# Kernel tuning notes

Hardware: AMD Instinct MI355X
Metric: run time of the kernel (lower is better)

## Reference

```python
import jax, jax.numpy as jnp
import numpy as np

SQRT_HALF = 1.0 / np.sqrt(2.0)


def _sep_filter(x, h, axis):
    """Depthwise 1D filter along `axis` (-1 = rows of the image i.e. horizontal,
    -2 = columns i.e. vertical) with symmetric boundary extension.
    x: (B, C, H, W); h: (m,) with m odd. Output has same spatial shape.
    Matches torch F.conv2d (cross-correlation) with groups=C on symmetric-padded input."""
    ch = x.shape[1]
    m = h.shape[0]
    p = m // 2
    if axis == -1:
        xe = jnp.pad(x, ((0, 0), (0, 0), (0, 0), (p, p)), mode='symmetric')
        k = jnp.tile(h.reshape(1, 1, 1, m), (ch, 1, 1, 1))
    else:
        xe = jnp.pad(x, ((0, 0), (0, 0), (p, p), (0, 0)), mode='symmetric')
        k = jnp.tile(h.reshape(1, 1, m, 1), (ch, 1, 1, 1))
    return jax.lax.conv_general_dilated(
        xe, k, window_strides=(1, 1), padding='VALID',
        dimension_numbers=('NCHW', 'OIHW', 'NCHW'), feature_group_count=ch)


def rowfilter(x, h):
    return _sep_filter(x, h, axis=-1)


def colfilter(x, h):
    return _sep_filter(x, h, axis=-2)


def q2c(y):
    """Quads -> two complex subimages. Returns (z1r, z1i, z2r, z2i),
    each (B, C, H/2, W/2)."""
    y = y * SQRT_HALF
    a = y[..., 0::2, 0::2]
    b = y[..., 0::2, 1::2]
    c = y[..., 1::2, 0::2]
    d = y[..., 1::2, 1::2]
    return a - d, b + c, a + d, b - c


def setup_inputs() -> dict:
    key = jax.random.key(0)
    k1, k2, k3 = jax.random.split(key, 3)
    B, C, H, W = 4, 32, 512, 512
    x = jax.random.normal(k1, (B, C, H, W), dtype=jnp.float32)
    h0o = jax.random.normal(k2, (5,), dtype=jnp.float32)  # near_sym_a lowpass: 5 taps
    h1o = jax.random.normal(k3, (7,), dtype=jnp.float32)  # near_sym_a highpass: 7 taps
    return {"input": x, "h0o": h0o, "h1o": h1o}


def reference(input, h0o, h1o):
    Lo = rowfilter(input, h0o)
    Hi = rowfilter(input, h1o)
    LoLo = colfilter(Lo, h0o)
    LoHi = colfilter(Lo, h1o)
    HiLo = colfilter(Hi, h0o)
    HiHi = colfilter(Hi, h1o)

    deg15r, deg15i, deg165r, deg165i = q2c(LoHi)
    deg45r, deg45i, deg135r, deg135i = q2c(HiHi)
    deg75r, deg75i, deg105r, deg105i = q2c(HiLo)

    Yhr = jnp.stack([deg15r, deg45r, deg75r, deg105r, deg135r, deg165r], axis=2)
    Yhi = jnp.stack([deg15i, deg45i, deg75i, deg105i, deg135i, deg165i], axis=2)
    Yl = LoLo
    return Yl, Yhr, Yhi
```

## Files before the change

### kernel.cpp

```cpp
#include <hip/hip_runtime.h>

#define H 512
#define W 512
#define NIMG 128
#define TH 16
#define TW 128
#define XR (TH + 6)
#define XC 136
#define XFLAT (XR * XC)
#define XPAD 3072
#define YSPLIT 4
#define NT (H / TH / YSPLIT)

#define YHR_OFF ((long)NIMG * H * W)
#define BSTRIDE ((long)(H / 2) * (W / 2))
#define YH_SIZE ((long)NIMG * 6 * BSTRIDE)
#define YHI_OFF (YHR_OFF + YH_SIZE)

__device__ __forceinline__ int reflect512(int g) {
    g = (g < 0) ? (-1 - g) : g;
    g = (g > H - 1) ? (2 * H - 1 - g) : g;
    return g;
}

__device__ __forceinline__ float4 f4fma(float s, float4 a, float4 acc) {
    acc.x = fmaf(s, a.x, acc.x);
    acc.y = fmaf(s, a.y, acc.y);
    acc.z = fmaf(s, a.z, acc.z);
    acc.w = fmaf(s, a.w, acc.w);
    return acc;
}

__global__ __launch_bounds__(256, 4)
void dtcwt_fwd1(const float* __restrict__ x,
                const float* __restrict__ h0o,
                const float* __restrict__ h1o,
                float* __restrict__ out)
{
    __shared__ __align__(16) float xin[XPAD];
    __shared__ __align__(16) float slo[XR][TW];
    __shared__ __align__(16) float shi[XR][TW];

    const int tid = threadIdx.x;
    const int x0 = blockIdx.x * TW;
    const int ys = blockIdx.y * (NT * TH);
    const int img = blockIdx.z;

    float c0[5], c1[7];
#pragma unroll
    for (int j = 0; j < 5; ++j) c0[j] = h0o[j];
#pragma unroll
    for (int j = 0; j < 7; ++j) c1[j] = h1o[j];

    const long ibase = (long)img * (H * W);
    float* __restrict__ yhr = out + YHR_OFF;
    float* __restrict__ yhi = out + YHI_OFF;
    const float sc = 0.70710678118654752440f;

    int sr[3]; int sst[3]; bool srev[3]; bool sact[3];
#pragma unroll
    for (int s = 0; s < 3; ++s) {
        int flat = tid * 4 + s * 1024;
        sact[s] = (flat < XFLAT);
        int r = flat / XC;
        int c = flat - r * XC;
        int g0 = x0 - 4 + c;
        int st = g0; bool rv = false;
        if (g0 < 0)          { st = -g0 - 4;        rv = true; }
        else if (g0 > W - 4) { st = 2 * W - 4 - g0; rv = true; }
        sr[s] = r; sst[s] = st; srev[s] = rv;
    }

    auto stage_issue = [&](int t, float4 v[3]) {
        const int yb = ys + t * TH - 3;
#pragma unroll
        for (int s = 0; s < 3; ++s) {
            if (!sact[s]) continue;
            const int gy = reflect512(yb + sr[s]);
            v[s] = *(const float4*)&x[ibase + (long)gy * W + sst[s]];
        }
    };
    auto stage_write = [&](float4 v[3]) {
#pragma unroll
        for (int s = 0; s < 3; ++s) {
            if (!sact[s]) continue;
            float4 w = v[s];
            if (srev[s]) w = make_float4(w.w, w.z, w.y, w.x);
            *(float4*)&xin[tid * 4 + s * 1024] = w;
        }
    };

    {
        float4 stg[3];
        stage_issue(0, stg);
        stage_write(stg);
    }
    __syncthreads();

    for (int t = 0; t < NT; ++t) {
        float4 nstg[3];
        if (t + 1 < NT) stage_issue(t + 1, nstg);

        for (int i = tid; i < XR * (TW / 4); i += 256) {
            int r = i >> 5;
            int w0 = (i & 31) * 4;
            const float* xr = &xin[r * XC];
            float4 A  = *(const float4*)&xr[w0];
            float4 Bv = *(const float4*)&xr[w0 + 4];
            float4 Cv = *(const float4*)&xr[w0 + 8];
            float f1 = A.y, f2 = A.z, f3 = A.w;
            float f4 = Bv.x, f5 = Bv.y, f6 = Bv.z, f7 = Bv.w;
            float f8 = Cv.x, f9 = Cv.y, f10 = Cv.z;
            float lo0 = c0[0]*f2 + c0[1]*f3 + c0[2]*f4 + c0[3]*f5 + c0[4]*f6;
            float lo1 = c0[0]*f3 + c0[1]*f4 + c0[2]*f5 + c0[3]*f6 + c0[4]*f7;
            float lo2 = c0[0]*f4 + c0[1]*f5 + c0[2]*f6 + c0[3]*f7 + c0[4]*f8;
            float lo3 = c0[0]*f5 + c0[1]*f6 + c0[2]*f7 + c0[3]*f8 + c0[4]*f9;
            float hi0 = c1[0]*f1 + c1[1]*f2 + c1[2]*f3 + c1[3]*f4 + c1[4]*f5 + c1[5]*f6 + c1[6]*f7;
            float hi1 = c1[0]*f2 + c1[1]*f3 + c1[2]*f4 + c1[3]*f5 + c1[4]*f6 + c1[5]*f7 + c1[6]*f8;
            float hi2 = c1[0]*f3 + c1[1]*f4 + c1[2]*f5 + c1[3]*f6 + c1[4]*f7 + c1[5]*f8 + c1[6]*f9;
            float hi3 = c1[0]*f4 + c1[1]*f5 + c1[2]*f6 + c1[3]*f7 + c1[4]*f8 + c1[5]*f9 + c1[6]*f10;
            *(float4*)&slo[r][w0] = make_float4(lo0, lo1, lo2, lo3);
            *(float4*)&shi[r][w0] = make_float4(hi0, hi1, hi2, hi3);
        }
        __syncthreads();

        {
            const int qr = tid >> 5;
            const int q4 = tid & 31;
            const int r0 = qr * 2;
            const int w0 = q4 * 4;
            const int yt = ys + t * TH;

            float4 L[8];
#pragma unroll
            for (int j = 0; j < 8; ++j) L[j] = *(const float4*)&slo[r0 + j][w0];

            float4 ll0 = make_float4(0.f, 0.f, 0.f, 0.f);
            float4 ll1 = ll0, lh0 = ll0, lh1 = ll0;
#pragma unroll
            for (int j = 0; j < 5; ++j) {
                ll0 = f4fma(c0[j], L[1 + j], ll0);
                ll1 = f4fma(c0[j], L[2 + j], ll1);
            }
#pragma unroll
            for (int j = 0; j < 7; ++j) {
                lh0 = f4fma(c1[j], L[j],     lh0);
                lh1 = f4fma(c1[j], L[1 + j], lh1);
            }

            const long ylb = ibase + (long)(yt + r0) * W + (x0 + w0);
            *(float4*)&out[ylb]     = ll0;
            *(float4*)&out[ylb + W] = ll1;

            float4 Hv[8];
#pragma unroll
            for (int j = 0; j < 8; ++j) Hv[j] = *(const float4*)&shi[r0 + j][w0];

            float4 hl0 = make_float4(0.f, 0.f, 0.f, 0.f);
            float4 hl1 = hl0, hh0 = hl0, hh1 = hl0;
#pragma unroll
            for (int j = 0; j < 5; ++j) {
                hl0 = f4fma(c0[j], Hv[1 + j], hl0);
                hl1 = f4fma(c0[j], Hv[2 + j], hl1);
            }
#pragma unroll
            for (int j = 0; j < 7; ++j) {
                hh0 = f4fma(c1[j], Hv[j],     hh0);
                hh1 = f4fma(c1[j], Hv[1 + j], hh1);
            }

            const int qy = (yt >> 1) + qr;
            const int qx = (x0 >> 1) + q4 * 2;
            const long hb = (long)img * 6 * BSTRIDE + (long)qy * (W / 2) + qx;

            *(float2*)&yhr[hb + 0 * BSTRIDE] = make_float2((lh0.x - lh1.y) * sc, (lh0.z - lh1.w) * sc);
            *(float2*)&yhi[hb + 0 * BSTRIDE] = make_float2((lh0.y + lh1.x) * sc, (lh0.w + lh1.z) * sc);
            *(float2*)&yhr[hb + 1 * BSTRIDE] = make_float2((hh0.x - hh1.y) * sc, (hh0.z - hh1.w) * sc);
            *(float2*)&yhi[hb + 1 * BSTRIDE] = make_float2((hh0.y + hh1.x) * sc, (hh0.w + hh1.z) * sc);
            *(float2*)&yhr[hb + 2 * BSTRIDE] = make_float2((hl0.x - hl1.y) * sc, (hl0.z - hl1.w) * sc);
            *(float2*)&yhi[hb + 2 * BSTRIDE] = make_float2((hl0.y + hl1.x) * sc, (hl0.w + hl1.z) * sc);
            *(float2*)&yhr[hb + 3 * BSTRIDE] = make_float2((hl0.x + hl1.y) * sc, (hl0.z + hl1.w) * sc);
            *(float2*)&yhi[hb + 3 * BSTRIDE] = make_float2((hl0.y - hl1.x) * sc, (hl0.w - hl1.z) * sc);
            *(float2*)&yhr[hb + 4 * BSTRIDE] = make_float2((hh0.x + hh1.y) * sc, (hh0.z + hh1.w) * sc);
            *(float2*)&yhi[hb + 4 * BSTRIDE] = make_float2((hh0.y - hh1.x) * sc, (hh0.w - hh1.z) * sc);
            *(float2*)&yhr[hb + 5 * BSTRIDE] = make_float2((lh0.x + lh1.y) * sc, (lh0.z + lh1.w) * sc);
            *(float2*)&yhi[hb + 5 * BSTRIDE] = make_float2((lh0.y - lh1.x) * sc, (lh0.w - lh1.z) * sc);
        }

        if (t + 1 < NT) stage_write(nstg);
        __syncthreads();
    }
}

extern "C" void kernel_launch(void* const* d_in, const int* in_sizes, int n_in,
                              void* d_out, int out_size, void* d_ws, size_t ws_size,
                              hipStream_t stream) {
    const float* x   = (const float*)d_in[0];
    const float* h0o = (const float*)d_in[1];
    const float* h1o = (const float*)d_in[2];
    float* out = (float*)d_out;
    dim3 grid(W / TW, YSPLIT, NIMG);
    dtcwt_fwd1<<<grid, dim3(256), 0, stream>>>(x, h0o, h1o, out);
}
```

Measured before the change: 662.5 us.

## Stage input tiles with direct global-to-LDS loads and separate halo buffer

Replaces register-staged float4 loads of the input tile with global_load_lds DMA into a dense interior LDS buffer, and loads the reflected horizontal halo separately as scalars into a small halo array. The next tile's interior load is issued after the row-filter sync so it overlaps with the column-filter and output-store phase. This removes register staging and the reversal shuffles for boundary chunks, but adds branchy halo selection in the row filter and relies on the async LDS writes completing before the end-of-iteration barrier (no explicit vmcnt wait is visible).

```diff
diff --git a/kernel.cpp b/kernel.cpp
--- a/kernel.cpp
+++ b/kernel.cpp
@@ -6,11 +6,11 @@
 #define TH 16
 #define TW 128
 #define XR (TH + 6)
-#define XC 136
-#define XFLAT (XR * XC)
-#define XPAD 3072
 #define YSPLIT 4
 #define NT (H / TH / YSPLIT)
+
+#define NCHUNK (XR * (TW / 4))
+#define NHALO  (XR * 8)
 
 #define YHR_OFF ((long)NIMG * H * W)
 #define BSTRIDE ((long)(H / 2) * (W / 2))
@@ -31,13 +31,18 @@
     return acc;
 }
 
+#define GLOAD_LDS16(g, l) __builtin_amdgcn_global_load_lds(                      \
+    (const __attribute__((address_space(1))) void*)(g),                          \
+    (__attribute__((address_space(3))) void*)(l), 16, 0, 0)
+
 __global__ __launch_bounds__(256, 4)
 void dtcwt_fwd1(const float* __restrict__ x,
                 const float* __restrict__ h0o,
                 const float* __restrict__ h1o,
                 float* __restrict__ out)
 {
-    __shared__ __align__(16) float xin[XPAD];
+    __shared__ __align__(16) float xint[XR][TW];
+    __shared__ __align__(16) float xhalo[XR][8];
     __shared__ __align__(16) float slo[XR][TW];
     __shared__ __align__(16) float shi[XR][TW];
 
@@ -57,57 +62,49 @@
     float* __restrict__ yhi = out + YHI_OFF;
     const float sc = 0.70710678118654752440f;
 
-    int sr[3]; int sst[3]; bool srev[3]; bool sact[3];
+    int   sr[3]; int sgx[3]; bool sact[3]; float* sdst[3];
 #pragma unroll
     for (int s = 0; s < 3; ++s) {
-        int flat = tid * 4 + s * 1024;
-        sact[s] = (flat < XFLAT);
-        int r = flat / XC;
-        int c = flat - r * XC;
-        int g0 = x0 - 4 + c;
-        int st = g0; bool rv = false;
-        if (g0 < 0)          { st = -g0 - 4;        rv = true; }
-        else if (g0 > W - 4) { st = 2 * W - 4 - g0; rv = true; }
-        sr[s] = r; sst[s] = st; srev[s] = rv;
+        int k = tid + 256 * s;
+        sact[s] = (k < NCHUNK);
+        sr[s]   = k >> 5;
+        sgx[s]  = x0 + 4 * (k & 31);
+        sdst[s] = &xint[0][0] + k * 4;
     }
-
-    auto stage_issue = [&](int t, float4 v[3]) {
+    const bool hact0 = (tid < NHALO);
+    const int  hr = tid >> 3;
+    const int  hj = tid & 7;
+    const int  hgx = reflect512((hj < 4) ? (x0 - 4 + hj) : (x0 + 124 + hj));
+
+    auto issue_interior = [&](int t) {
         const int yb = ys + t * TH - 3;
 #pragma unroll
         for (int s = 0; s < 3; ++s) {
             if (!sact[s]) continue;
             const int gy = reflect512(yb + sr[s]);
-            v[s] = *(const float4*)&x[ibase + (long)gy * W + sst[s]];
+            GLOAD_LDS16(&x[ibase + (long)gy * W + sgx[s]], sdst[s]);
         }
     };
-    auto stage_write = [&](float4 v[3]) {
-#pragma unroll
-        for (int s = 0; s < 3; ++s) {
-            if (!sact[s]) continue;
-            float4 w = v[s];
-            if (srev[s]) w = make_float4(w.w, w.z, w.y, w.x);
-            *(float4*)&xin[tid * 4 + s * 1024] = w;
-        }
-    };
-
-    {
-        float4 stg[3];
-        stage_issue(0, stg);
-        stage_write(stg);
-    }
+
+    issue_interior(0);
+    if (hact0) xhalo[hr][hj] = x[ibase + (long)reflect512(ys - 3 + hr) * W + hgx];
     __syncthreads();
 
     for (int t = 0; t < NT; ++t) {
-        float4 nstg[3];
-        if (t + 1 < NT) stage_issue(t + 1, nstg);
+        const bool hact = hact0 && (t + 1 < NT);
+        float hreg = 0.f;
+        if (hact)
+            hreg = x[ibase + (long)reflect512(ys + (t + 1) * TH - 3 + hr) * W + hgx];
 
         for (int i = tid; i < XR * (TW / 4); i += 256) {
             int r = i >> 5;
             int w0 = (i & 31) * 4;
-            const float* xr = &xin[r * XC];
-            float4 A  = *(const float4*)&xr[w0];
-            float4 Bv = *(const float4*)&xr[w0 + 4];
-            float4 Cv = *(const float4*)&xr[w0 + 8];
+            const float* rowi = &xint[r][0];
+            const float* pa = (w0 == 0)   ? &xhalo[r][0] : rowi + (w0 - 4);
+            const float* pc = (w0 == 124) ? &xhalo[r][4] : rowi + (w0 + 4);
+            float4 A  = *(const float4*)pa;
+            float4 Bv = *(const float4*)(rowi + w0);
+            float4 Cv = *(const float4*)pc;
             float f1 = A.y, f2 = A.z, f3 = A.w;
             float f4 = Bv.x, f5 = Bv.y, f6 = Bv.z, f7 = Bv.w;
             float f8 = Cv.x, f9 = Cv.y, f10 = Cv.z;
@@ -124,6 +121,11 @@
         }
         __syncthreads();
 
+        if (t + 1 < NT) {
+            issue_interior(t + 1);
+            if (hact) xhalo[hr][hj] = hreg;
+        }
+
         {
             const int qr = tid >> 5;
             const int q4 = tid & 31;
@@ -187,7 +189,6 @@
             *(float2*)&yhi[hb + 5 * BSTRIDE] = make_float2((lh0.y - lh1.x) * sc, (lh0.w - lh1.z) * sc);
         }
 
-        if (t + 1 < NT) stage_write(nstg);
         __syncthreads();
     }
 }
```

Measured after the change: 626.6 us. -5.4%, faster.

## Replace shared-memory tiling with register sliding window over full-width rows

Applied to the files above, without the earlier changes.

Each 128-thread block now covers a full 512-wide row band, and each thread holds an 8-row ring buffer of row-filtered results in registers. Rows are streamed in with global float4 loads, neighbour columns are read straight from global or L1, and the two edge threads handle mirror boundaries. This drops shared memory and all __syncthreads, and cuts the vertical halo overhead by using taller bands. In exchange it uses more registers, has less parallelism (16x128 blocks of 128 threads), does redundant neighbour loads, and relies on the compiler keeping the ring-buffer indexing in registers after full unrolling.

```diff
diff --git a/kernel.cpp b/kernel.cpp
--- a/kernel.cpp
+++ b/kernel.cpp
@@ -3,14 +3,8 @@
 #define H 512
 #define W 512
 #define NIMG 128
-#define TH 16
-#define TW 128
-#define XR (TH + 6)
-#define XC 136
-#define XFLAT (XR * XC)
-#define XPAD 3072
-#define YSPLIT 4
-#define NT (H / TH / YSPLIT)
+#define NBAND 16
+#define BR (H / NBAND)
 
 #define YHR_OFF ((long)NIMG * H * W)
 #define BSTRIDE ((long)(H / 2) * (W / 2))
@@ -31,20 +25,33 @@
     return acc;
 }
 
-__global__ __launch_bounds__(256, 4)
+__device__ __forceinline__ void rowcomp(float4 A, float4 Bv, float4 C,
+                                        const float* c0, const float* c1,
+                                        float4& lo, float4& hi) {
+    float f1 = A.y, f2 = A.z, f3 = A.w;
+    float f4 = Bv.x, f5 = Bv.y, f6 = Bv.z, f7 = Bv.w;
+    float f8 = C.x, f9 = C.y, f10 = C.z;
+    lo.x = c0[0]*f2 + c0[1]*f3 + c0[2]*f4 + c0[3]*f5 + c0[4]*f6;
+    lo.y = c0[0]*f3 + c0[1]*f4 + c0[2]*f5 + c0[3]*f6 + c0[4]*f7;
+    lo.z = c0[0]*f4 + c0[1]*f5 + c0[2]*f6 + c0[3]*f7 + c0[4]*f8;
+    lo.w = c0[0]*f5 + c0[1]*f6 + c0[2]*f7 + c0[3]*f8 + c0[4]*f9;
+    hi.x = c1[0]*f1 + c1[1]*f2 + c1[2]*f3 + c1[3]*f4 + c1[4]*f5 + c1[5]*f6 + c1[6]*f7;
+    hi.y = c1[0]*f2 + c1[1]*f3 + c1[2]*f4 + c1[3]*f5 + c1[4]*f6 + c1[5]*f7 + c1[6]*f8;
+    hi.z = c1[0]*f3 + c1[1]*f4 + c1[2]*f5 + c1[3]*f6 + c1[4]*f7 + c1[5]*f8 + c1[6]*f9;
+    hi.w = c1[0]*f4 + c1[1]*f5 + c1[2]*f6 + c1[3]*f7 + c1[4]*f8 + c1[5]*f9 + c1[6]*f10;
+}
+
+__global__ __launch_bounds__(128, 3)
 void dtcwt_fwd1(const float* __restrict__ x,
                 const float* __restrict__ h0o,
                 const float* __restrict__ h1o,
                 float* __restrict__ out)
 {
-    __shared__ __align__(16) float xin[XPAD];
-    __shared__ __align__(16) float slo[XR][TW];
-    __shared__ __align__(16) float shi[XR][TW];
-
-    const int tid = threadIdx.x;
-    const int x0 = blockIdx.x * TW;
-    const int ys = blockIdx.y * (NT * TH);
-    const int img = blockIdx.z;
+    const int t   = threadIdx.x;
+    const int cg  = t * 4;
+    const int ys  = blockIdx.x * BR;
+    const int img = blockIdx.y;
+    const bool e0 = (t == 0), e1 = (t == 127);
 
     float c0[5], c1[7];
 #pragma unroll
@@ -53,142 +60,105 @@
     for (int j = 0; j < 7; ++j) c1[j] = h1o[j];
 
     const long ibase = (long)img * (H * W);
-    float* __restrict__ yhr = out + YHR_OFF;
-    float* __restrict__ yhi = out + YHI_OFF;
+    const float* __restrict__ xi = x + ibase;
+    float* __restrict__ yl  = out + ibase;
+    float* __restrict__ yhr = out + YHR_OFF + (long)img * 6 * BSTRIDE;
+    float* __restrict__ yhi = out + YHI_OFF + (long)img * 6 * BSTRIDE;
     const float sc = 0.70710678118654752440f;
 
-    int sr[3]; int sst[3]; bool srev[3]; bool sact[3];
+    float4 wlo[8], whi[8];
+
 #pragma unroll
-    for (int s = 0; s < 3; ++s) {
-        int flat = tid * 4 + s * 1024;
-        sact[s] = (flat < XFLAT);
-        int r = flat / XC;
-        int c = flat - r * XC;
-        int g0 = x0 - 4 + c;
-        int st = g0; bool rv = false;
-        if (g0 < 0)          { st = -g0 - 4;        rv = true; }
-        else if (g0 > W - 4) { st = 2 * W - 4 - g0; rv = true; }
-        sr[s] = r; sst[s] = st; srev[s] = rv;
+    for (int p = 0; p < 8; ++p) {
+        const float* rp = xi + (long)reflect512(ys - 3 + p) * W + cg;
+        float4 Bv = *(const float4*)rp;
+        float4 Ar = *(const float4*)(e0 ? rp : rp - 4);
+        float4 Cr = *(const float4*)(e1 ? rp : rp + 4);
+        float4 rB = make_float4(Bv.w, Bv.z, Bv.y, Bv.x);
+        float4 Av = e0 ? rB : Ar;
+        float4 Cv = e1 ? rB : Cr;
+        rowcomp(Av, Bv, Cv, c0, c1, wlo[p], whi[p]);
     }
 
-    auto stage_issue = [&](int t, float4 v[3]) {
-        const int yb = ys + t * TH - 3;
+    for (int qo = 0; qo < 4; ++qo) {
 #pragma unroll
-        for (int s = 0; s < 3; ++s) {
-            if (!sact[s]) continue;
-            const int gy = reflect512(yb + sr[s]);
-            v[s] = *(const float4*)&x[ibase + (long)gy * W + sst[s]];
-        }
-    };
-    auto stage_write = [&](float4 v[3]) {
-#pragma unroll
-        for (int s = 0; s < 3; ++s) {
-            if (!sact[s]) continue;
-            float4 w = v[s];
-            if (srev[s]) w = make_float4(w.w, w.z, w.y, w.x);
-            *(float4*)&xin[tid * 4 + s * 1024] = w;
-        }
-    };
+        for (int qi = 0; qi < 4; ++qi) {
+            const int q   = qo * 4 + qi;
+            const int yr0 = ys + 2 * q;
+            const int b0  = (2 * qi) & 7;
+            const int b1  = (b0 + 1) & 7;
 
-    {
-        float4 stg[3];
-        stage_issue(0, stg);
-        stage_write(stg);
-    }
-    __syncthreads();
+            const float* rp0 = xi + (long)reflect512(yr0 + 5) * W + cg;
+            const float* rp1 = xi + (long)reflect512(yr0 + 6) * W + cg;
+            float4 B0 = *(const float4*)rp0;
+            float4 A0r = *(const float4*)(e0 ? rp0 : rp0 - 4);
+            float4 C0r = *(const float4*)(e1 ? rp0 : rp0 + 4);
+            float4 B1 = *(const float4*)rp1;
+            float4 A1r = *(const float4*)(e0 ? rp1 : rp1 - 4);
+            float4 C1r = *(const float4*)(e1 ? rp1 : rp1 + 4);
 
-    for (int t = 0; t < NT; ++t) {
-        float4 nstg[3];
-        if (t + 1 < NT) stage_issue(t + 1, nstg);
-
-        for (int i = tid; i < XR * (TW / 4); i += 256) {
-            int r = i >> 5;
-            int w0 = (i & 31) * 4;
-            const float* xr = &xin[r * XC];
-            float4 A  = *(const float4*)&xr[w0];
-            float4 Bv = *(const float4*)&xr[w0 + 4];
-            float4 Cv = *(const float4*)&xr[w0 + 8];
-            float f1 = A.y, f2 = A.z, f3 = A.w;
-            float f4 = Bv.x, f5 = Bv.y, f6 = Bv.z, f7 = Bv.w;
-            float f8 = Cv.x, f9 = Cv.y, f10 = Cv.z;
-            float lo0 = c0[0]*f2 + c0[1]*f3 + c0[2]*f4 + c0[3]*f5 + c0[4]*f6;
-            float lo1 = c0[0]*f3 + c0[1]*f4 + c0[2]*f5 + c0[3]*f6 + c0[4]*f7;
-            float lo2 = c0[0]*f4 + c0[1]*f5 + c0[2]*f6 + c0[3]*f7 + c0[4]*f8;
-            float lo3 = c0[0]*f5 + c0[1]*f6 + c0[2]*f7 + c0[3]*f8 + c0[4]*f9;
-            float hi0 = c1[0]*f1 + c1[1]*f2 + c1[2]*f3 + c1[3]*f4 + c1[4]*f5 + c1[5]*f6 + c1[6]*f7;
-            float hi1 = c1[0]*f2 + c1[1]*f3 + c1[2]*f4 + c1[3]*f5 + c1[4]*f6 + c1[5]*f7 + c1[6]*f8;
-            float hi2 = c1[0]*f3 + c1[1]*f4 + c1[2]*f5 + c1[3]*f6 + c1[4]*f7 + c1[5]*f8 + c1[6]*f9;
-            float hi3 = c1[0]*f4 + c1[1]*f5 + c1[2]*f6 + c1[3]*f7 + c1[4]*f8 + c1[5]*f9 + c1[6]*f10;
-            *(float4*)&slo[r][w0] = make_float4(lo0, lo1, lo2, lo3);
-            *(float4*)&shi[r][w0] = make_float4(hi0, hi1, hi2, hi3);
-        }
-        __syncthreads();
-
-        {
-            const int qr = tid >> 5;
-            const int q4 = tid & 31;
-            const int r0 = qr * 2;
-            const int w0 = q4 * 4;
-            const int yt = ys + t * TH;
-
-            float4 L[8];
-#pragma unroll
-            for (int j = 0; j < 8; ++j) L[j] = *(const float4*)&slo[r0 + j][w0];
-
-            float4 ll0 = make_float4(0.f, 0.f, 0.f, 0.f);
-            float4 ll1 = ll0, lh0 = ll0, lh1 = ll0;
+            float4 ll0 = make_float4(0.f, 0.f, 0.f, 0.f), ll1 = ll0;
 #pragma unroll
             for (int j = 0; j < 5; ++j) {
-                ll0 = f4fma(c0[j], L[1 + j], ll0);
-                ll1 = f4fma(c0[j], L[2 + j], ll1);
+                ll0 = f4fma(c0[j], wlo[(b0 + 1 + j) & 7], ll0);
+                ll1 = f4fma(c0[j], wlo[(b0 + 2 + j) & 7], ll1);
             }
-#pragma unroll
-            for (int j = 0; j < 7; ++j) {
-                lh0 = f4fma(c1[j], L[j],     lh0);
-                lh1 = f4fma(c1[j], L[1 + j], lh1);
+            {
+                const long ylb = (long)yr0 * W + cg;
+                *(float4*)&yl[ylb]     = ll0;
+                *(float4*)&yl[ylb + W] = ll1;
             }
 
-            const long ylb = ibase + (long)(yt + r0) * W + (x0 + w0);
-            *(float4*)&out[ylb]     = ll0;
-            *(float4*)&out[ylb + W] = ll1;
+            const long hb = (long)(yr0 >> 1) * (W / 2) + 2 * t;
 
-            float4 Hv[8];
+            {
+                float4 lh0 = make_float4(0.f, 0.f, 0.f, 0.f), lh1 = lh0;
 #pragma unroll
-            for (int j = 0; j < 8; ++j) Hv[j] = *(const float4*)&shi[r0 + j][w0];
-
-            float4 hl0 = make_float4(0.f, 0.f, 0.f, 0.f);
-            float4 hl1 = hl0, hh0 = hl0, hh1 = hl0;
+                for (int j = 0; j < 7; ++j) {
+                    lh0 = f4fma(c1[j], wlo[(b0 + j) & 7],     lh0);
+                    lh1 = f4fma(c1[j], wlo[(b0 + 1 + j) & 7], lh1);
+                }
+                *(float2*)&yhr[hb + 0 * BSTRIDE] = make_float2((lh0.x - lh1.y) * sc, (lh0.z - lh1.w) * sc);
+                *(float2*)&yhi[hb + 0 * BSTRIDE] = make_float2((lh0.y + lh1.x) * sc, (lh0.w + lh1.z) * sc);
+                *(float2*)&yhr[hb + 5 * BSTRIDE] = make_float2((lh0.x + lh1.y) * sc, (lh0.z + lh1.w) * sc);
+                *(float2*)&yhi[hb + 5 * BSTRIDE] = make_float2((lh0.y - lh1.x) * sc, (lh0.w - lh1.z) * sc);
+            }
+            {
+                float4 hl0 = make_float4(0.f, 0.f, 0.f, 0.f), hl1 = hl0;
 #pragma unroll
-            for (int j = 0; j < 5; ++j) {
-                hl0 = f4fma(c0[j], Hv[1 + j], hl0);
-                hl1 = f4fma(c0[j], Hv[2 + j], hl1);
+                for (int j = 0; j < 5; ++j) {
+                    hl0 = f4fma(c0[j], whi[(b0 + 1 + j) & 7], hl0);
+                    hl1 = f4fma(c0[j], whi[(b0 + 2 + j) & 7], hl1);
+                }
+                *(float2*)&yhr[hb + 2 * BSTRIDE] = make_float2((hl0.x - hl1.y) * sc, (hl0.z - hl1.w) * sc);
+                *(float2*)&yhi[hb + 2 * BSTRIDE] = make_float2((hl0.y + hl1.x) * sc, (hl0.w + hl1.z) * sc);
+                *(float2*)&yhr[hb + 3 * BSTRIDE] = make_float2((hl0.x + hl1.y) * sc, (hl0.z + hl1.w) * sc);
+                *(float2*)&yhi[hb + 3 * BSTRIDE] = make_float2((hl0.y - hl1.x) * sc, (hl0.w - hl1.z) * sc);
             }
+            {
+                float4 hh0 = make_float4(0.f, 0.f, 0.f, 0.f), hh1 = hh0;
 #pragma unroll
-            for (int j = 0; j < 7; ++j) {
-                hh0 = f4fma(c1[j], Hv[j],     hh0);
-                hh1 = f4fma(c1[j], Hv[1 + j], hh1);
+                for (int j = 0; j < 7; ++j) {
+                    hh0 = f4fma(c1[j], whi[(b0 + j) & 7],     hh0);
+                    hh1 = f4fma(c1[j], whi[(b0 + 1 + j) & 7], hh1);
+                }
+                *(float2*)&yhr[hb + 1 * BSTRIDE] = make_float2((hh0.x - hh1.y) * sc, (hh0.z - hh1.w) * sc);
+                *(float2*)&yhi[hb + 1 * BSTRIDE] = make_float2((hh0.y + hh1.x) * sc, (hh0.w + hh1.z) * sc);
+                *(float2*)&yhr[hb + 4 * BSTRIDE] = make_float2((hh0.x + hh1.y) * sc, (hh0.z + hh1.w) * sc);
+                *(float2*)&yhi[hb + 4 * BSTRIDE] = make_float2((hh0.y - hh1.x) * sc, (hh0.w - hh1.z) * sc);
             }
 
-            const int qy = (yt >> 1) + qr;
-            const int qx = (x0 >> 1) + q4 * 2;
-            const long hb = (long)img * 6 * BSTRIDE + (long)qy * (W / 2) + qx;
-
-            *(float2*)&yhr[hb + 0 * BSTRIDE] = make_float2((lh0.x - lh1.y) * sc, (lh0.z - lh1.w) * sc);
-            *(float2*)&yhi[hb + 0 * BSTRIDE] = make_float2((lh0.y + lh1.x) * sc, (lh0.w + lh1.z) * sc);
-            *(float2*)&yhr[hb + 1 * BSTRIDE] = make_float2((hh0.x - hh1.y) * sc, (hh0.z - hh1.w) * sc);
-            *(float2*)&yhi[hb + 1 * BSTRIDE] = make_float2((hh0.y + hh1.x) * sc, (hh0.w + hh1.z) * sc);
-            *(float2*)&yhr[hb + 2 * BSTRIDE] = make_float2((hl0.x - hl1.y) * sc, (hl0.z - hl1.w) * sc);
-            *(float2*)&yhi[hb + 2 * BSTRIDE] = make_float2((hl0.y + hl1.x) * sc, (hl0.w + hl1.z) * sc);
-            *(float2*)&yhr[hb + 3 * BSTRIDE] = make_float2((hl0.x + hl1.y) * sc, (hl0.z + hl1.w) * sc);
-            *(float2*)&yhi[hb + 3 * BSTRIDE] = make_float2((hl0.y - hl1.x) * sc, (hl0.w - hl1.z) * sc);
-            *(float2*)&yhr[hb + 4 * BSTRIDE] = make_float2((hh0.x + hh1.y) * sc, (hh0.z + hh1.w) * sc);
-            *(float2*)&yhi[hb + 4 * BSTRIDE] = make_float2((hh0.y - hh1.x) * sc, (hh0.w - hh1.z) * sc);
-            *(float2*)&yhr[hb + 5 * BSTRIDE] = make_float2((lh0.x + lh1.y) * sc, (lh0.z + lh1.w) * sc);
-            *(float2*)&yhi[hb + 5 * BSTRIDE] = make_float2((lh0.y - lh1.x) * sc, (lh0.w - lh1.z) * sc);
+            {
+                float4 rB0 = make_float4(B0.w, B0.z, B0.y, B0.x);
+                float4 A0 = e0 ? rB0 : A0r;
+                float4 C0 = e1 ? rB0 : C0r;
+                rowcomp(A0, B0, C0, c0, c1, wlo[b0], whi[b0]);
+                float4 rB1 = make_float4(B1.w, B1.z, B1.y, B1.x);
+                float4 A1 = e0 ? rB1 : A1r;
+                float4 C1 = e1 ? rB1 : C1r;
+                rowcomp(A1, B1, C1, c0, c1, wlo[b1], whi[b1]);
+            }
         }
-
-        if (t + 1 < NT) stage_write(nstg);
-        __syncthreads();
     }
 }
 
@@ -199,6 +169,6 @@
     const float* h0o = (const float*)d_in[1];
     const float* h1o = (const float*)d_in[2];
     float* out = (float*)d_out;
-    dim3 grid(W / TW, YSPLIT, NIMG);
-    dtcwt_fwd1<<<grid, dim3(256), 0, stream>>>(x, h0o, h1o, out);
+    dim3 grid(NBAND, NIMG);
+    dtcwt_fwd1<<<grid, dim3(128), 0, stream>>>(x, h0o, h1o, out);
 }
```

New measurement: 666.4 us. About the same (+0.6%).
